# Kernel optimization log

Measured on AMD Instinct MI355X. Metric: run time of the kernel, lower is better.

## Reference

```python
import math
import jax, jax.numpy as jnp
import numpy as np

B, S, D, H = 1, 4096, 1024, 16
HD = D // H


def setup_inputs() -> dict:
    key = jax.random.key(0)
    ks = jax.random.split(key, 11)
    s = 0.02
    inp = {
        "q": jax.random.normal(ks[0], (B, S, D), jnp.float32),
        "k": jax.random.normal(ks[1], (B, S, D), jnp.float32),
        "v": jax.random.normal(ks[2], (B, S, D), jnp.float32),
        # causal boolean mask, broadcastable over [B, H, S, S]
        "mask": jnp.tril(jnp.ones((S, S), jnp.bool_))[None, None],
        "Wq": jax.random.normal(ks[3], (D, D), jnp.float32) * s,
        "bq": jnp.zeros((D,), jnp.float32),
        "Wk": jax.random.normal(ks[4], (D, D), jnp.float32) * s,
        "bk": jnp.zeros((D,), jnp.float32),
        "Wv": jax.random.normal(ks[5], (D, D), jnp.float32) * s,
        "bv": jnp.zeros((D,), jnp.float32),
        "Wo": jax.random.normal(ks[6], (D, D), jnp.float32) * s,
        "bo": jnp.zeros((D,), jnp.float32),
    }
    return inp


def reference(q, k, v, mask, Wq, bq, Wk, bk, Wv, bv, Wo, bo):
    # projections (torch Linear: x @ W.T + b; here W is stored already transposed)
    qp = (q @ Wq + bq).reshape(B, S, H, HD)
    kp = (k @ Wk + bk).reshape(B, S, H, HD)
    vp = (v @ Wv + bv).reshape(B, S, H, HD)
    # scores: [B, H, S, S]
    scores = jnp.einsum("bqhd,bkhd->bhqk", qp, kp) / math.sqrt(HD)
    scores = jnp.where(mask, scores, -jnp.inf)
    attn = jax.nn.softmax(scores, axis=-1)
    # context: [B, H, S, HD] -> [B, S, D]
    ctx = jnp.einsum("bhqk,bkhd->bqhd", attn, vp).reshape(B, S, D)
    return ctx @ Wo + bo
```

## Files before the change

### kernel.cpp

```cpp
#include <hip/hip_runtime.h>
#include <hip/hip_bf16.h>


#define S_LEN 4096
#define D_DIM 1024
#define NHEAD 16
#define HDIM  64

typedef __hip_bfloat16 bf16;
typedef __attribute__((ext_vector_type(8))) short bf16x8v;
typedef __attribute__((ext_vector_type(4))) float f32x4;

#define MFMA16(a, b, c) __builtin_amdgcn_mfma_f32_16x16x32_bf16((a), (b), (c), 0, 0, 0)

#if __has_builtin(__builtin_amdgcn_exp2f)
#define EXP2F(x) __builtin_amdgcn_exp2f(x)
#else
#define EXP2F(x) exp2f(x)
#endif

#define QSCALE (0.125f * 1.4426950408889634f)

__device__ __forceinline__ void async_cp16(const void* g, void* l) {
    __builtin_amdgcn_global_load_lds(
        (const __attribute__((address_space(1))) unsigned int*)g,
        (__attribute__((address_space(3))) unsigned int*)l, 16, 0, 0);
}

__global__ __launch_bounds__(256) void cvt_bf16_k(
    const float* __restrict__ x0, const float* __restrict__ x1,
    const float* __restrict__ x2,
    bf16* __restrict__ y0, bf16* __restrict__ y1, bf16* __restrict__ y2)
{
    const float* x = (blockIdx.z == 0) ? x0 : (blockIdx.z == 1) ? x1 : x2;
    bf16*       y = (blockIdx.z == 0) ? y0 : (blockIdx.z == 1) ? y1 : y2;
    const size_t i = ((size_t)blockIdx.x * 256 + threadIdx.x);
    const float4 v = ((const float4*)x)[i];
    union { bf16 h[4]; short4 s; } u;
    u.h[0] = __float2bfloat16(v.x);
    u.h[1] = __float2bfloat16(v.y);
    u.h[2] = __float2bfloat16(v.z);
    u.h[3] = __float2bfloat16(v.w);
    ((short4*)y)[i] = u.s;
}

__global__ __launch_bounds__(256) void transpose_cvt_k(
    const float* __restrict__ W0, const float* __restrict__ W1,
    const float* __restrict__ W2, const float* __restrict__ W3,
    bf16* __restrict__ T0, bf16* __restrict__ T1,
    bf16* __restrict__ T2, bf16* __restrict__ T3)
{
    const float* W = (blockIdx.z == 0) ? W0 : (blockIdx.z == 1) ? W1
                   : (blockIdx.z == 2) ? W2 : W3;
    bf16*       Wt = (blockIdx.z == 0) ? T0 : (blockIdx.z == 1) ? T1
                   : (blockIdx.z == 2) ? T2 : T3;
    __shared__ float t[32][33];
    const int bx = blockIdx.x << 5, by = blockIdx.y << 5;
    const int tx = threadIdx.x & 31, ty = threadIdx.x >> 5;
#pragma unroll
    for (int i = 0; i < 32; i += 8)
        t[ty + i][tx] = W[(size_t)(by + ty + i) * D_DIM + bx + tx];
    __syncthreads();
#pragma unroll
    for (int i = 0; i < 32; i += 8)
        Wt[(size_t)(bx + ty + i) * D_DIM + by + tx] = __float2bfloat16(t[tx][ty + i]);
}

struct GemmJob {
    const bf16* A; const bf16* Wt; const float* bias; void* out;
    int mode; float scale;
};

__global__ __launch_bounds__(256) void gemm_k(GemmJob j0, GemmJob j1, GemmJob j2)
{
    const GemmJob j = (blockIdx.z == 0) ? j0 : (blockIdx.z == 1) ? j1 : j2;
    const int K = D_DIM;
    const int bn = blockIdx.x << 7;
    const int bm = blockIdx.y << 7;
    const int tid = threadIdx.x;
    const int w = tid >> 6, lane = tid & 63;
    const int col = lane & 15, g = lane >> 4;
    const int wr = (w >> 1) << 6, wc = (w & 1) << 6;

    __shared__ bf16 As[128 * 64];
    __shared__ bf16 Bs[128 * 64];

    f32x4 acc[4][4];
#pragma unroll
    for (int i = 0; i < 4; ++i)
#pragma unroll
        for (int jj = 0; jj < 4; ++jj) acc[i][jj] = (f32x4){0.f, 0.f, 0.f, 0.f};

    for (int kb = 0; kb < K; kb += 64) {
        __syncthreads();
#pragma unroll
        for (int e = 0; e < 4; ++e) {
            const int lin = (e << 8) + tid;
            const int row = lin >> 3, kc = lin & 7;
            async_cp16(j.A + (size_t)(bm + row) * K + kb + (kc << 3), &As[lin << 3]);
        }
#pragma unroll
        for (int e = 0; e < 4; ++e) {
            const int lin = (e << 8) + tid;
            const int row = lin >> 3, kc = lin & 7;
            async_cp16(j.Wt + (size_t)(bn + row) * K + kb + (kc << 3), &Bs[lin << 3]);
        }
        __syncthreads();

#pragma unroll
        for (int s = 0; s < 2; ++s) {
            bf16x8v af[4], bfv[4];
#pragma unroll
            for (int i = 0; i < 4; ++i)
                af[i] = *(const bf16x8v*)&As[((wr + (i << 4) + col) << 6) + (s << 5) + (g << 3)];
#pragma unroll
            for (int jj = 0; jj < 4; ++jj)
                bfv[jj] = *(const bf16x8v*)&Bs[((wc + (jj << 4) + col) << 6) + (s << 5) + (g << 3)];
#pragma unroll
            for (int i = 0; i < 4; ++i)
#pragma unroll
                for (int jj = 0; jj < 4; ++jj)
                    acc[i][jj] = MFMA16(af[i], bfv[jj], acc[i][jj]);
        }
    }

#pragma unroll
    for (int i = 0; i < 4; ++i)
#pragma unroll
    for (int jj = 0; jj < 4; ++jj)
#pragma unroll
    for (int reg = 0; reg < 4; ++reg) {
        const int row = bm + wr + (i << 4) + (g << 2) + reg;
        const int cg  = bn + wc + (jj << 4) + col;
        const float vv = (acc[i][jj][reg] + j.bias[cg]) * j.scale;
        if (j.mode == 0)
            ((bf16*)j.out)[(((size_t)(cg >> 6)) * S_LEN + row) * HDIM + (cg & 63)] =
                __float2bfloat16(vv);
        else if (j.mode == 2)
            ((bf16*)j.out)[((size_t)(cg >> 6) * HDIM + (cg & 63)) * S_LEN + row] =
                __float2bfloat16(vv);
        else
            ((float*)j.out)[(size_t)row * D_DIM + cg] = vv;
    }
}

__global__ __launch_bounds__(256) void attn_mfma_k(
    const bf16* __restrict__ Qp, const bf16* __restrict__ Kp,
    const bf16* __restrict__ Vt, bf16* __restrict__ ctx)
{
    __shared__ bf16 Ks[2][4096];
    __shared__ bf16 Vs[2][4096];
    __shared__ bf16 Ps[4][1024];

    const int bid = blockIdx.x;
    const int qb  = 63 - (bid >> 4);
    const int h   = bid & 15;
    const int q0  = qb << 6;
    const int tid = threadIdx.x, w = tid >> 6, lane = tid & 63;
    const int col = lane & 15, g = lane >> 4;

    const bf16* Kh = Kp + (size_t)h * S_LEN * HDIM;
    const bf16* Vh = Vt + (size_t)h * HDIM * S_LEN;

    const size_t qrow_base = ((size_t)h * S_LEN + q0 + (w << 4) + col) * HDIM + (g << 3);
    const bf16x8v qf0 = *(const bf16x8v*)(Qp + qrow_base);
    const bf16x8v qf1 = *(const bf16x8v*)(Qp + qrow_base + 32);

    const int sig_r = (col >> 2) | (((col & 3) ^ (g & 1)) << 2);
    const int pr0 = (((g) << 4) | sig_r) << 3;
    const int pr1 = (((4 + g) << 4) | sig_r) << 3;
    int pw[4][4];
#pragma unroll
    for (int t = 0; t < 4; ++t) {
        const int Gw = (t << 1) + (col >> 3);
#pragma unroll
        for (int reg = 0; reg < 4; ++reg) {
            const int sig = g | (((reg ^ (Gw & 1)) & 3) << 2);
            pw[t][reg] = (((Gw << 4) | sig) << 3) + (col & 7);
        }
    }

    float pl[4] = {0.f, 0.f, 0.f, 0.f};
    f32x4 acco[4];
#pragma unroll
    for (int t = 0; t < 4; ++t) acco[t] = (f32x4){0.f, 0.f, 0.f, 0.f};

    const int nkb = qb + 1;

    auto stage = [&](int buf, int kb) {
        const int kk0 = kb << 6;
#pragma unroll
        for (int e = 0; e < 2; ++e) {
            const int lin = (e << 8) + tid;
            const int t = lin >> 7, G = (lin >> 4) & 7, c = lin & 15;
            async_cp16(Kh + (size_t)(kk0 + (t << 4) + c) * HDIM + (G << 3),
                       &Ks[buf][lin << 3]);
            async_cp16(Vh + (size_t)((t << 4) + c) * S_LEN + kk0 + (G << 3),
                       &Vs[buf][lin << 3]);
        }
    };

    stage(0, 0);
    __syncthreads();

    for (int kb = 0; kb < nkb; ++kb) {
        const int cur = kb & 1;
        if (kb + 1 < nkb) stage(cur ^ 1, kb + 1);
        const int kk0 = kb << 6;
        const bf16* Kc = Ks[cur];
        const bf16* Vc = Vs[cur];

        f32x4 sa[4];
#pragma unroll
        for (int t = 0; t < 4; ++t) sa[t] = (f32x4){0.f, 0.f, 0.f, 0.f};
#pragma unroll
        for (int t = 0; t < 4; ++t) {
            sa[t] = MFMA16(qf0, *(const bf16x8v*)&Kc[((t << 7) + (g << 4) + col) << 3], sa[t]);
            sa[t] = MFMA16(qf1, *(const bf16x8v*)&Kc[((t << 7) + 64 + (g << 4) + col) << 3], sa[t]);
        }

        const bool lastt = (kb == nkb - 1);
#pragma unroll
        for (int t = 0; t < 4; ++t) {
#pragma unroll
            for (int reg = 0; reg < 4; ++reg) {
                float p;
                if (lastt && (kk0 + (t << 4) + col > q0 + (w << 4) + (g << 2) + reg))
                    p = 0.f;
                else
                    p = EXP2F(sa[t][reg]);
                pl[reg] += p;
                Ps[w][pw[t][reg]] = __float2bfloat16(p);
            }
        }

        const bf16x8v pf0 = *(const bf16x8v*)&Ps[w][pr0];
        const bf16x8v pf1 = *(const bf16x8v*)&Ps[w][pr1];
#pragma unroll
        for (int t = 0; t < 4; ++t) {
            acco[t] = MFMA16(pf0, *(const bf16x8v*)&Vc[((t << 7) + (g << 4) + col) << 3], acco[t]);
            acco[t] = MFMA16(pf1, *(const bf16x8v*)&Vc[((t << 7) + 64 + (g << 4) + col) << 3], acco[t]);
        }

        __syncthreads();
    }

    float lrow[4];
#pragma unroll
    for (int reg = 0; reg < 4; ++reg) {
        float l = pl[reg];
        l += __shfl_xor(l, 1);
        l += __shfl_xor(l, 2);
        l += __shfl_xor(l, 4);
        l += __shfl_xor(l, 8);
        lrow[reg] = l;
    }

#pragma unroll
    for (int t = 0; t < 4; ++t)
#pragma unroll
        for (int reg = 0; reg < 4; ++reg) {
            const int row = q0 + (w << 4) + (g << 2) + reg;
            ctx[(size_t)row * D_DIM + h * HDIM + (t << 4) + col] =
                __float2bfloat16(acco[t][reg] / lrow[reg]);
        }
}

extern "C" void kernel_launch(void* const* d_in, const int* in_sizes, int n_in,
                              void* d_out, int out_size, void* d_ws, size_t ws_size,
                              hipStream_t stream)
{
    const float* q  = (const float*)d_in[0];
    const float* k  = (const float*)d_in[1];
    const float* v  = (const float*)d_in[2];
    const float* Wq = (const float*)d_in[4];
    const float* bq = (const float*)d_in[5];
    const float* Wk = (const float*)d_in[6];
    const float* bk = (const float*)d_in[7];
    const float* Wv = (const float*)d_in[8];
    const float* bv = (const float*)d_in[9];
    const float* Wo = (const float*)d_in[10];
    const float* bo = (const float*)d_in[11];

    const size_t PE  = (size_t)S_LEN * D_DIM;
    const size_t WTE = (size_t)D_DIM * D_DIM;

    const dim3 tg(32, 32, 4);
    const dim3 gg(D_DIM / 128, S_LEN / 128, 1);
    const dim3 gg3(D_DIM / 128, S_LEN / 128, 3);
    const dim3 cg((unsigned)(PE / 1024), 1, 3);

    if (ws_size >= (size_t)64 * 1024 * 1024) {
        bf16* Qb = (bf16*)d_ws;
        bf16* Kb = Qb + PE;
        bf16* Vb = Kb + PE;
        bf16* Qp = Vb + PE;
        bf16* Kp = Qp + PE;
        bf16* Vt = Kp + PE;
        bf16* Wtq = Vt + PE;
        bf16* Wtk = Wtq + WTE;
        bf16* Wtv = Wtk + WTE;
        bf16* Wto = Wtv + WTE;
        bf16* ctx = Qb;

        transpose_cvt_k<<<tg, 256, 0, stream>>>(Wq, Wk, Wv, Wo, Wtq, Wtk, Wtv, Wto);
        cvt_bf16_k<<<cg, 256, 0, stream>>>(q, k, v, Qb, Kb, Vb);

        GemmJob jq{Qb, Wtq, bq, Qp, 0, QSCALE};
        GemmJob jk{Kb, Wtk, bk, Kp, 0, 1.0f};
        GemmJob jv{Vb, Wtv, bv, Vt, 2, 1.0f};
        gemm_k<<<gg3, 256, 0, stream>>>(jq, jk, jv);

        attn_mfma_k<<<dim3(1024), 256, 0, stream>>>(Qp, Kp, Vt, ctx);

        GemmJob jo{ctx, Wto, bo, d_out, 1, 1.0f};
        gemm_k<<<gg, 256, 0, stream>>>(jo, jo, jo);
    } else {
        bf16* X  = (bf16*)d_ws;
        bf16* Qp = X + PE;
        bf16* Kp = Qp + PE;
        bf16* Vt = Kp + PE;
        bf16* Wtq = Vt + PE;
        bf16* Wtk = Wtq + WTE;
        bf16* Wtv = Wtk + WTE;
        bf16* Wto = Wtv + WTE;

        transpose_cvt_k<<<tg, 256, 0, stream>>>(Wq, Wk, Wv, Wo, Wtq, Wtk, Wtv, Wto);

        const dim3 cg1((unsigned)(PE / 1024), 1, 1);
        cvt_bf16_k<<<cg1, 256, 0, stream>>>(q, q, q, X, X, X);
        GemmJob jq{X, Wtq, bq, Qp, 0, QSCALE};
        gemm_k<<<gg, 256, 0, stream>>>(jq, jq, jq);
        cvt_bf16_k<<<cg1, 256, 0, stream>>>(k, k, k, X, X, X);
        GemmJob jk{X, Wtk, bk, Kp, 0, 1.0f};
        gemm_k<<<gg, 256, 0, stream>>>(jk, jk, jk);
        cvt_bf16_k<<<cg1, 256, 0, stream>>>(v, v, v, X, X, X);
        GemmJob jv{X, Wtv, bv, Vt, 2, 1.0f};
        gemm_k<<<gg, 256, 0, stream>>>(jv, jv, jv);

        attn_mfma_k<<<dim3(1024), 256, 0, stream>>>(Qp, Kp, Vt, X);

        GemmJob jo{X, Wto, bo, d_out, 1, 1.0f};
        gemm_k<<<gg, 256, 0, stream>>>(jo, jo, jo);
    }
}
```

Measured before the change: 355.4 us.

## Keep attention probabilities in registers via permlane swaps; narrow GEMM tiles

The attention kernel now computes S transposed (K as the A operand), so each lane holds a column of scores for its own query row. It packs them with v_cvt_pk_bf16_f32 and redistributes them with permlane32/16 swaps instead of a round trip through LDS, which also simplifies the row-sum reduction and allows vectorized output stores. MFMA sections get s_setprio hints. The projection GEMM tile shrinks from 128x128 to 128x64, doubling the block count for more occupancy and parallelism at the cost of less operand reuse per block.

After: 322.9 us. 1.1x faster.

```diff
diff --git a/kernel.cpp b/kernel.cpp
--- a/kernel.cpp
+++ b/kernel.cpp
@@ -10,6 +10,7 @@
 typedef __hip_bfloat16 bf16;
 typedef __attribute__((ext_vector_type(8))) short bf16x8v;
 typedef __attribute__((ext_vector_type(4))) float f32x4;
+typedef __attribute__((ext_vector_type(2))) unsigned int u32x2;
 
 #define MFMA16(a, b, c) __builtin_amdgcn_mfma_f32_16x16x32_bf16((a), (b), (c), 0, 0, 0)
 
@@ -25,6 +26,12 @@
     __builtin_amdgcn_global_load_lds(
         (const __attribute__((address_space(1))) unsigned int*)g,
         (__attribute__((address_space(3))) unsigned int*)l, 16, 0, 0);
+}
+
+__device__ __forceinline__ unsigned int cvtpk_bf16(float lo, float hi) {
+    unsigned int r;
+    asm("v_cvt_pk_bf16_f32 %0, %1, %2" : "=v"(r) : "v"(lo), "v"(hi));
+    return r;
 }
 
 __global__ __launch_bounds__(256) void cvt_bf16_k(
@@ -75,21 +82,21 @@
 {
     const GemmJob j = (blockIdx.z == 0) ? j0 : (blockIdx.z == 1) ? j1 : j2;
     const int K = D_DIM;
-    const int bn = blockIdx.x << 7;
+    const int bn = blockIdx.x << 6;
     const int bm = blockIdx.y << 7;
     const int tid = threadIdx.x;
     const int w = tid >> 6, lane = tid & 63;
     const int col = lane & 15, g = lane >> 4;
-    const int wr = (w >> 1) << 6, wc = (w & 1) << 6;
+    const int wr = (w >> 1) << 6, wc = (w & 1) << 5;
 
     __shared__ bf16 As[128 * 64];
-    __shared__ bf16 Bs[128 * 64];
-
-    f32x4 acc[4][4];
+    __shared__ bf16 Bs[64 * 64];
+
+    f32x4 acc[4][2];
 #pragma unroll
     for (int i = 0; i < 4; ++i)
 #pragma unroll
-        for (int jj = 0; jj < 4; ++jj) acc[i][jj] = (f32x4){0.f, 0.f, 0.f, 0.f};
+        for (int jj = 0; jj < 2; ++jj) acc[i][jj] = (f32x4){0.f, 0.f, 0.f, 0.f};
 
     for (int kb = 0; kb < K; kb += 64) {
         __syncthreads();
@@ -100,7 +107,7 @@
             async_cp16(j.A + (size_t)(bm + row) * K + kb + (kc << 3), &As[lin << 3]);
         }
 #pragma unroll
-        for (int e = 0; e < 4; ++e) {
+        for (int e = 0; e < 2; ++e) {
             const int lin = (e << 8) + tid;
             const int row = lin >> 3, kc = lin & 7;
             async_cp16(j.Wt + (size_t)(bn + row) * K + kb + (kc << 3), &Bs[lin << 3]);
@@ -109,17 +116,17 @@
 
 #pragma unroll
         for (int s = 0; s < 2; ++s) {
-            bf16x8v af[4], bfv[4];
+            bf16x8v af[4], bfv[2];
 #pragma unroll
             for (int i = 0; i < 4; ++i)
                 af[i] = *(const bf16x8v*)&As[((wr + (i << 4) + col) << 6) + (s << 5) + (g << 3)];
 #pragma unroll
-            for (int jj = 0; jj < 4; ++jj)
+            for (int jj = 0; jj < 2; ++jj)
                 bfv[jj] = *(const bf16x8v*)&Bs[((wc + (jj << 4) + col) << 6) + (s << 5) + (g << 3)];
 #pragma unroll
             for (int i = 0; i < 4; ++i)
 #pragma unroll
-                for (int jj = 0; jj < 4; ++jj)
+                for (int jj = 0; jj < 2; ++jj)
                     acc[i][jj] = MFMA16(af[i], bfv[jj], acc[i][jj]);
         }
     }
@@ -127,7 +134,7 @@
 #pragma unroll
     for (int i = 0; i < 4; ++i)
 #pragma unroll
-    for (int jj = 0; jj < 4; ++jj)
+    for (int jj = 0; jj < 2; ++jj)
 #pragma unroll
     for (int reg = 0; reg < 4; ++reg) {
         const int row = bm + wr + (i << 4) + (g << 2) + reg;
@@ -150,7 +157,6 @@
 {
     __shared__ bf16 Ks[2][4096];
     __shared__ bf16 Vs[2][4096];
-    __shared__ bf16 Ps[4][1024];
 
     const int bid = blockIdx.x;
     const int qb  = 63 - (bid >> 4);
@@ -162,25 +168,12 @@
     const bf16* Kh = Kp + (size_t)h * S_LEN * HDIM;
     const bf16* Vh = Vt + (size_t)h * HDIM * S_LEN;
 
-    const size_t qrow_base = ((size_t)h * S_LEN + q0 + (w << 4) + col) * HDIM + (g << 3);
+    const int qrow = q0 + (w << 4) + col;
+    const size_t qrow_base = ((size_t)h * S_LEN + qrow) * HDIM + (g << 3);
     const bf16x8v qf0 = *(const bf16x8v*)(Qp + qrow_base);
     const bf16x8v qf1 = *(const bf16x8v*)(Qp + qrow_base + 32);
 
-    const int sig_r = (col >> 2) | (((col & 3) ^ (g & 1)) << 2);
-    const int pr0 = (((g) << 4) | sig_r) << 3;
-    const int pr1 = (((4 + g) << 4) | sig_r) << 3;
-    int pw[4][4];
-#pragma unroll
-    for (int t = 0; t < 4; ++t) {
-        const int Gw = (t << 1) + (col >> 3);
-#pragma unroll
-        for (int reg = 0; reg < 4; ++reg) {
-            const int sig = g | (((reg ^ (Gw & 1)) & 3) << 2);
-            pw[t][reg] = (((Gw << 4) | sig) << 3) + (col & 7);
-        }
-    }
-
-    float pl[4] = {0.f, 0.f, 0.f, 0.f};
+    float pl = 0.f;
     f32x4 acco[4];
 #pragma unroll
     for (int t = 0; t < 4; ++t) acco[t] = (f32x4){0.f, 0.f, 0.f, 0.f};
@@ -213,57 +206,76 @@
         f32x4 sa[4];
 #pragma unroll
         for (int t = 0; t < 4; ++t) sa[t] = (f32x4){0.f, 0.f, 0.f, 0.f};
+        __builtin_amdgcn_s_setprio(1);
 #pragma unroll
         for (int t = 0; t < 4; ++t) {
-            sa[t] = MFMA16(qf0, *(const bf16x8v*)&Kc[((t << 7) + (g << 4) + col) << 3], sa[t]);
-            sa[t] = MFMA16(qf1, *(const bf16x8v*)&Kc[((t << 7) + 64 + (g << 4) + col) << 3], sa[t]);
-        }
+            sa[t] = MFMA16(*(const bf16x8v*)&Kc[((t << 7) + (g << 4) + col) << 3], qf0, sa[t]);
+            sa[t] = MFMA16(*(const bf16x8v*)&Kc[((t << 7) + 64 + (g << 4) + col) << 3], qf1, sa[t]);
+        }
+        __builtin_amdgcn_s_setprio(0);
 
         const bool lastt = (kb == nkb - 1);
 #pragma unroll
         for (int t = 0; t < 4; ++t) {
 #pragma unroll
             for (int reg = 0; reg < 4; ++reg) {
+                const int kidx = kk0 + (t << 4) + (g << 2) + reg;
                 float p;
-                if (lastt && (kk0 + (t << 4) + col > q0 + (w << 4) + (g << 2) + reg))
+                if (lastt && kidx > qrow)
                     p = 0.f;
                 else
                     p = EXP2F(sa[t][reg]);
-                pl[reg] += p;
-                Ps[w][pw[t][reg]] = __float2bfloat16(p);
+                pl += p;
+                sa[t][reg] = p;
             }
         }
 
-        const bf16x8v pf0 = *(const bf16x8v*)&Ps[w][pr0];
-        const bf16x8v pf1 = *(const bf16x8v*)&Ps[w][pr1];
+        unsigned int c0[4], c1[4];
 #pragma unroll
         for (int t = 0; t < 4; ++t) {
-            acco[t] = MFMA16(pf0, *(const bf16x8v*)&Vc[((t << 7) + (g << 4) + col) << 3], acco[t]);
-            acco[t] = MFMA16(pf1, *(const bf16x8v*)&Vc[((t << 7) + 64 + (g << 4) + col) << 3], acco[t]);
-        }
+            c0[t] = cvtpk_bf16(sa[t][0], sa[t][1]);
+            c1[t] = cvtpk_bf16(sa[t][2], sa[t][3]);
+        }
+        union { unsigned int wd[4]; bf16x8v v; } pb0, pb1;
+        {
+            u32x2 r0 = __builtin_amdgcn_permlane32_swap(c0[0], c0[1], false, false);
+            u32x2 r1 = __builtin_amdgcn_permlane32_swap(c1[0], c1[1], false, false);
+            u32x2 s0 = __builtin_amdgcn_permlane16_swap(r0[0], r0[1], false, false);
+            u32x2 s1 = __builtin_amdgcn_permlane16_swap(r1[0], r1[1], false, false);
+            pb0.wd[0] = s0[0]; pb0.wd[1] = s1[0]; pb0.wd[2] = s0[1]; pb0.wd[3] = s1[1];
+        }
+        {
+            u32x2 r0 = __builtin_amdgcn_permlane32_swap(c0[2], c0[3], false, false);
+            u32x2 r1 = __builtin_amdgcn_permlane32_swap(c1[2], c1[3], false, false);
+            u32x2 s0 = __builtin_amdgcn_permlane16_swap(r0[0], r0[1], false, false);
+            u32x2 s1 = __builtin_amdgcn_permlane16_swap(r1[0], r1[1], false, false);
+            pb1.wd[0] = s0[0]; pb1.wd[1] = s1[0]; pb1.wd[2] = s0[1]; pb1.wd[3] = s1[1];
+        }
+
+        __builtin_amdgcn_s_setprio(1);
+#pragma unroll
+        for (int t = 0; t < 4; ++t) {
+            acco[t] = MFMA16(*(const bf16x8v*)&Vc[((t << 7) + (g << 4) + col) << 3], pb0.v, acco[t]);
+            acco[t] = MFMA16(*(const bf16x8v*)&Vc[((t << 7) + 64 + (g << 4) + col) << 3], pb1.v, acco[t]);
+        }
+        __builtin_amdgcn_s_setprio(0);
 
         __syncthreads();
     }
 
-    float lrow[4];
-#pragma unroll
-    for (int reg = 0; reg < 4; ++reg) {
-        float l = pl[reg];
-        l += __shfl_xor(l, 1);
-        l += __shfl_xor(l, 2);
-        l += __shfl_xor(l, 4);
-        l += __shfl_xor(l, 8);
-        lrow[reg] = l;
-    }
-
-#pragma unroll
-    for (int t = 0; t < 4; ++t)
-#pragma unroll
-        for (int reg = 0; reg < 4; ++reg) {
-            const int row = q0 + (w << 4) + (g << 2) + reg;
-            ctx[(size_t)row * D_DIM + h * HDIM + (t << 4) + col] =
-                __float2bfloat16(acco[t][reg] / lrow[reg]);
-        }
+    float l = pl;
+    l += __shfl_xor(l, 16);
+    l += __shfl_xor(l, 32);
+    const float inv = 1.f / l;
+
+#pragma unroll
+    for (int t = 0; t < 4; ++t) {
+        union { bf16 hh[4]; short4 s4; } u;
+#pragma unroll
+        for (int reg = 0; reg < 4; ++reg)
+            u.hh[reg] = __float2bfloat16(acco[t][reg] * inv);
+        *(short4*)&ctx[(size_t)qrow * D_DIM + h * HDIM + (t << 4) + (g << 2)] = u.s4;
+    }
 }
 
 extern "C" void kernel_launch(void* const* d_in, const int* in_sizes, int n_in,
@@ -286,8 +298,8 @@
     const size_t WTE = (size_t)D_DIM * D_DIM;
 
     const dim3 tg(32, 32, 4);
-    const dim3 gg(D_DIM / 128, S_LEN / 128, 1);
-    const dim3 gg3(D_DIM / 128, S_LEN / 128, 3);
+    const dim3 gg(D_DIM / 64, S_LEN / 128, 1);
+    const dim3 gg3(D_DIM / 64, S_LEN / 128, 3);
     const dim3 cg((unsigned)(PE / 1024), 1, 3);
 
     if (ws_size >= (size_t)64 * 1024 * 1024) {
```
